# Kernel tuning notes

Hardware: AMD Instinct MI355X
Metric: run time of the kernel (lower is better)

Reference implementation:

```python
import jax, jax.numpy as jnp
import numpy as np

# Irrep dims for irreps 0e, 1o, 2e: 2l+1
IRREP_DIMS = (1, 3, 5)
B, N, C_IN, C_OUT = 8, 4096, 256, 256
FEAT = sum(IRREP_DIMS)  # 9


def setup_inputs() -> dict:
    key = jax.random.key(0)
    kx, k0, k1, k2 = jax.random.split(key, 4)
    std = C_IN ** -0.5  # VarianceScaling(fan_in) init
    return {
        "x": jax.random.normal(kx, (B, N, C_IN, FEAT), dtype=jnp.float32),
        "w0": jax.random.normal(k0, (C_IN, C_OUT), dtype=jnp.float32) * std,
        "w1": jax.random.normal(k1, (C_IN, C_OUT), dtype=jnp.float32) * std,
        "w2": jax.random.normal(k2, (C_IN, C_OUT), dtype=jnp.float32) * std,
    }


def reference(x, w0, w1, w2):
    # EquivariantLinear with mix_channels=True:
    #  - axis_to_mul merges the channel axis into irrep multiplicity, so each
    #    irrep block x[..., k, m] (k = channel/mul index, m = 2l+1 component)
    #    is contracted over k with a per-irrep weight w_l [mul_in, mul_out],
    #    scaled by path_weight = 1/sqrt(fan_in) (single path per output irrep).
    #  - mul_to_axis splits the multiplicity back into the channel axis.
    # Block-diagonal structure: one small matmul per matching irrep pair.
    mul_in = x.shape[-2]
    pw = jnp.asarray(mul_in, x.dtype) ** -0.5  # path_weight (1/sqrt fan_in)
    outs = []
    offset = 0
    for w, d in zip((w0, w1, w2), IRREP_DIMS):
        xl = jax.lax.slice_in_dim(x, offset, offset + d, axis=-1)  # [B,N,C,d]
        outs.append(pw * jnp.einsum('bnkm,kc->bncm', xl, w))
        offset += d
    return jnp.concatenate(outs, axis=-1)  # [B, N, C_out, 9]
```

## Files before the change

kernel.cpp:

```cpp
#include <hip/hip_runtime.h>


typedef float f32x4 __attribute__((ext_vector_type(4)));
typedef short s16x8 __attribute__((ext_vector_type(8)));

#define POSB 16
#define XS_KS 264
#define XS_MS (POSB * XS_KS)
#define SMEM_BYTES (9 * XS_MS * 2)
#define STG_ROW 148

__device__ __forceinline__ unsigned short f2bf(float f) {
  unsigned u = __float_as_uint(f);
  return (unsigned short)((u + 0x7FFFu + ((u >> 16) & 1u)) >> 16);
}

__global__ void prep_w(const float* __restrict__ w0, const float* __restrict__ w1,
                       const float* __restrict__ w2, unsigned short* __restrict__ wt) {
  const int b = blockIdx.x;
  const int irr = b / 16;
  const int tile = b % 16;
  const int k0 = (tile >> 2) << 6;
  const int c0 = (tile & 3) << 6;
  const float* w = (irr == 0) ? w0 : ((irr == 1) ? w1 : w2);
  __shared__ float lt[64 * 65];
  const int t = threadIdx.x;
#pragma unroll
  for (int i = 0; i < 16; ++i) {
    int e = t + (i << 8);
    int kk = e >> 6, cc = e & 63;
    lt[cc * 65 + kk] = w[(k0 + kk) * 256 + (c0 + cc)];
  }
  __syncthreads();
#pragma unroll
  for (int i = 0; i < 16; ++i) {
    int e = t + (i << 8);
    int cc = e >> 6, kk = e & 63;
    wt[irr * 65536 + (c0 + cc) * 256 + (k0 + kk)] = f2bf(lt[cc * 65 + kk] * 0.0625f);
  }
}

__global__ __launch_bounds__(512, 4) void eqlin_main(
    const float* __restrict__ x, const unsigned short* __restrict__ wt,
    float* __restrict__ out) {
  extern __shared__ char smem[];
  unsigned short* xs = reinterpret_cast<unsigned short*>(smem);

  const int t = threadIdx.x;
  const long long blk = blockIdx.x;
  const float* xb = x + blk * (POSB * 2304);

#pragma unroll
  for (int i = 0; i < 2; ++i) {
    const int p = t + (i << 9);
    const int pos = p >> 6;
    const int kq = (p & 63) << 2;
    const f32x4* src = reinterpret_cast<const f32x4*>(xb) + p * 9;
    float f[36];
#pragma unroll
    for (int j = 0; j < 9; ++j) {
      f32x4 v = src[j];
      f[j * 4 + 0] = v[0]; f[j * 4 + 1] = v[1];
      f[j * 4 + 2] = v[2]; f[j * 4 + 3] = v[3];
    }
#pragma unroll
    for (int m = 0; m < 9; ++m) {
      unsigned long long pk =
          (unsigned long long)f2bf(f[m]) |
          ((unsigned long long)f2bf(f[9 + m]) << 16) |
          ((unsigned long long)f2bf(f[18 + m]) << 32) |
          ((unsigned long long)f2bf(f[27 + m]) << 48);
      *reinterpret_cast<unsigned long long*>(xs + m * XS_MS + pos * XS_KS + kq) = pk;
    }
  }
  __syncthreads();

  const int w = t >> 6;
  const int l = t & 63;
  const int cr = l & 15;
  const int kg = (l >> 4) << 3;
  const int c0 = w << 5;

  const unsigned short* xsA = xs + cr * XS_KS + kg;
  const unsigned short* wtB = wt + (c0 + cr) * 256 + kg;

  f32x4 accA[4][2];
#pragma unroll
  for (int m = 0; m < 4; ++m)
#pragma unroll
    for (int ct = 0; ct < 2; ++ct) accA[m][ct] = (f32x4){0.f, 0.f, 0.f, 0.f};

#pragma unroll 2
  for (int ks = 0; ks < 8; ++ks) {
    const int kk = ks << 5;
    s16x8 b00 = *reinterpret_cast<const s16x8*>(wtB + kk);
    s16x8 b01 = *reinterpret_cast<const s16x8*>(wtB + 4096 + kk);
    s16x8 b10 = *reinterpret_cast<const s16x8*>(wtB + 65536 + kk);
    s16x8 b11 = *reinterpret_cast<const s16x8*>(wtB + 65536 + 4096 + kk);
    {
      s16x8 a = *reinterpret_cast<const s16x8*>(xsA + kk);
      accA[0][0] = __builtin_amdgcn_mfma_f32_16x16x32_bf16(a, b00, accA[0][0], 0, 0, 0);
      accA[0][1] = __builtin_amdgcn_mfma_f32_16x16x32_bf16(a, b01, accA[0][1], 0, 0, 0);
    }
#pragma unroll
    for (int m = 1; m < 4; ++m) {
      s16x8 a = *reinterpret_cast<const s16x8*>(xsA + m * XS_MS + kk);
      accA[m][0] = __builtin_amdgcn_mfma_f32_16x16x32_bf16(a, b10, accA[m][0], 0, 0, 0);
      accA[m][1] = __builtin_amdgcn_mfma_f32_16x16x32_bf16(a, b11, accA[m][1], 0, 0, 0);
    }
  }

  f32x4 accB[5][2];
#pragma unroll
  for (int m = 0; m < 5; ++m)
#pragma unroll
    for (int ct = 0; ct < 2; ++ct) accB[m][ct] = (f32x4){0.f, 0.f, 0.f, 0.f};

#pragma unroll 2
  for (int ks = 0; ks < 8; ++ks) {
    const int kk = ks << 5;
    s16x8 b20 = *reinterpret_cast<const s16x8*>(wtB + 2 * 65536 + kk);
    s16x8 b21 = *reinterpret_cast<const s16x8*>(wtB + 2 * 65536 + 4096 + kk);
#pragma unroll
    for (int m = 0; m < 5; ++m) {
      s16x8 a = *reinterpret_cast<const s16x8*>(xsA + (m + 4) * XS_MS + kk);
      accB[m][0] = __builtin_amdgcn_mfma_f32_16x16x32_bf16(a, b20, accB[m][0], 0, 0, 0);
      accB[m][1] = __builtin_amdgcn_mfma_f32_16x16x32_bf16(a, b21, accB[m][1], 0, 0, 0);
    }
  }
  __syncthreads();

  float* stgw = reinterpret_cast<float*>(smem) + w * (POSB * STG_ROW);
  const int posb = (l >> 4) << 2;
  f32x4* o4 = reinterpret_cast<f32x4*>(out) + blk * 9216 + w * 72;

#pragma unroll
  for (int ct = 0; ct < 2; ++ct) {
#pragma unroll
    for (int m = 0; m < 9; ++m) {
#pragma unroll
      for (int j = 0; j < 4; ++j) {
        float v = (m < 4) ? accA[m][ct][j] : accB[m - 4][ct][j];
        stgw[(posb + j) * STG_ROW + cr * 9 + m] = v;
      }
    }
    asm volatile("s_waitcnt lgkmcnt(0)" ::: "memory");
#pragma unroll
    for (int q = 0; q < 9; ++q) {
      const int e = l + (q << 6);
      const int pos = (int)((unsigned)e / 36u);
      const int rem = e - pos * 36;
      f32x4 v = *reinterpret_cast<const f32x4*>(stgw + pos * STG_ROW + (rem << 2));
      o4[pos * 576 + ct * 36 + rem] = v;
    }
    asm volatile("s_waitcnt lgkmcnt(0)" ::: "memory");
  }
}

extern "C" void kernel_launch(void* const* d_in, const int* in_sizes, int n_in,
                              void* d_out, int out_size, void* d_ws, size_t ws_size,
                              hipStream_t stream) {
  const float* x = (const float*)d_in[0];
  const float* w0 = (const float*)d_in[1];
  const float* w1 = (const float*)d_in[2];
  const float* w2 = (const float*)d_in[3];
  unsigned short* wt = (unsigned short*)d_ws;
  float* out = (float*)d_out;

  prep_w<<<48, 256, 0, stream>>>(w0, w1, w2, wt);

  (void)hipFuncSetAttribute(reinterpret_cast<const void*>(eqlin_main),
                            hipFuncAttributeMaxDynamicSharedMemorySize, SMEM_BYTES);
  eqlin_main<<<2048, 512, SMEM_BYTES, stream>>>(x, wt, out);
}
```

Before: 184.3 us.

## Make main kernel persistent with double-buffered LDS and register prefetch of next tile

Launches 256 blocks that each loop over 8 position tiles instead of 2048 one-shot blocks. The next tile's fp32 input is loaded into registers while the current tile is computed and stored, then converted to bf16 into an alternate LDS buffer. This aims to overlap global loads with MFMA work and output stores and to amortise per-block startup. It doubles LDS use per block and adds prefetch registers, lowering occupancy.

```diff
diff --git a/kernel.cpp b/kernel.cpp
--- a/kernel.cpp
+++ b/kernel.cpp
@@ -7,8 +7,10 @@
 #define POSB 16
 #define XS_KS 264
 #define XS_MS (POSB * XS_KS)
-#define SMEM_BYTES (9 * XS_MS * 2)
+#define BUF_BYTES (9 * XS_MS * 2)
+#define SMEM_BYTES (2 * BUF_BYTES)
 #define STG_ROW 148
+#define TILES_PER_BLK 8
 
 __device__ __forceinline__ unsigned short f2bf(float f) {
   unsigned u = __float_as_uint(f);
@@ -40,120 +42,150 @@
   }
 }
 
-__global__ __launch_bounds__(512, 4) void eqlin_main(
+__device__ __forceinline__ void stage_unit(unsigned short* xs, int pos, int kq,
+                                           const f32x4* pf) {
+#pragma unroll
+  for (int m = 0; m < 9; ++m) {
+    unsigned long long pk =
+        (unsigned long long)f2bf(pf[m >> 2][m & 3]) |
+        ((unsigned long long)f2bf(pf[(9 + m) >> 2][(9 + m) & 3]) << 16) |
+        ((unsigned long long)f2bf(pf[(18 + m) >> 2][(18 + m) & 3]) << 32) |
+        ((unsigned long long)f2bf(pf[(27 + m) >> 2][(27 + m) & 3]) << 48);
+    *reinterpret_cast<unsigned long long*>(xs + m * XS_MS + pos * XS_KS + kq) = pk;
+  }
+}
+
+__global__ __launch_bounds__(512, 2) void eqlin_main(
     const float* __restrict__ x, const unsigned short* __restrict__ wt,
     float* __restrict__ out) {
   extern __shared__ char smem[];
-  unsigned short* xs = reinterpret_cast<unsigned short*>(smem);
 
   const int t = threadIdx.x;
-  const long long blk = blockIdx.x;
-  const float* xb = x + blk * (POSB * 2304);
-
-#pragma unroll
-  for (int i = 0; i < 2; ++i) {
-    const int p = t + (i << 9);
-    const int pos = p >> 6;
-    const int kq = (p & 63) << 2;
-    const f32x4* src = reinterpret_cast<const f32x4*>(xb) + p * 9;
-    float f[36];
-#pragma unroll
-    for (int j = 0; j < 9; ++j) {
-      f32x4 v = src[j];
-      f[j * 4 + 0] = v[0]; f[j * 4 + 1] = v[1];
-      f[j * 4 + 2] = v[2]; f[j * 4 + 3] = v[3];
-    }
-#pragma unroll
-    for (int m = 0; m < 9; ++m) {
-      unsigned long long pk =
-          (unsigned long long)f2bf(f[m]) |
-          ((unsigned long long)f2bf(f[9 + m]) << 16) |
-          ((unsigned long long)f2bf(f[18 + m]) << 32) |
-          ((unsigned long long)f2bf(f[27 + m]) << 48);
-      *reinterpret_cast<unsigned long long*>(xs + m * XS_MS + pos * XS_KS + kq) = pk;
-    }
-  }
-  __syncthreads();
+
+  const int pos0 = t >> 6;
+  const int pos1 = pos0 + 8;
+  const int kq = (t & 63) << 2;
+  const int u0 = t * 9;
+  const int u1 = (t + 512) * 9;
+
+  const f32x4* xg = reinterpret_cast<const f32x4*>(x);
 
   const int w = t >> 6;
   const int l = t & 63;
   const int cr = l & 15;
   const int kg = (l >> 4) << 3;
   const int c0 = w << 5;
-
-  const unsigned short* xsA = xs + cr * XS_KS + kg;
   const unsigned short* wtB = wt + (c0 + cr) * 256 + kg;
 
-  f32x4 accA[4][2];
-#pragma unroll
-  for (int m = 0; m < 4; ++m)
-#pragma unroll
-    for (int ct = 0; ct < 2; ++ct) accA[m][ct] = (f32x4){0.f, 0.f, 0.f, 0.f};
+  const long long tile0 = (long long)blockIdx.x * TILES_PER_BLK;
+
+  f32x4 pfA[9], pfB[9];
+
+  {
+    const f32x4* s = xg + tile0 * 9216;
+#pragma unroll
+    for (int j = 0; j < 9; ++j) pfA[j] = s[u0 + j];
+#pragma unroll
+    for (int j = 0; j < 9; ++j) pfB[j] = s[u1 + j];
+    unsigned short* xs0 = reinterpret_cast<unsigned short*>(smem);
+    stage_unit(xs0, pos0, kq, pfA);
+    stage_unit(xs0, pos1, kq, pfB);
+  }
+  __syncthreads();
+
+  for (int it = 0; it < TILES_PER_BLK; ++it) {
+    const int p = it & 1;
+    const unsigned short* xsb =
+        reinterpret_cast<const unsigned short*>(smem + p * BUF_BYTES);
+
+    if (it + 1 < TILES_PER_BLK) {
+      const f32x4* s = xg + (tile0 + it + 1) * 9216;
+#pragma unroll
+      for (int j = 0; j < 9; ++j) pfA[j] = s[u0 + j];
+#pragma unroll
+      for (int j = 0; j < 9; ++j) pfB[j] = s[u1 + j];
+    }
+
+    const unsigned short* xsA = xsb + cr * XS_KS + kg;
+
+    f32x4 accA[4][2];
+#pragma unroll
+    for (int m = 0; m < 4; ++m)
+#pragma unroll
+      for (int ct = 0; ct < 2; ++ct) accA[m][ct] = (f32x4){0.f, 0.f, 0.f, 0.f};
 
 #pragma unroll 2
-  for (int ks = 0; ks < 8; ++ks) {
-    const int kk = ks << 5;
-    s16x8 b00 = *reinterpret_cast<const s16x8*>(wtB + kk);
-    s16x8 b01 = *reinterpret_cast<const s16x8*>(wtB + 4096 + kk);
-    s16x8 b10 = *reinterpret_cast<const s16x8*>(wtB + 65536 + kk);
-    s16x8 b11 = *reinterpret_cast<const s16x8*>(wtB + 65536 + 4096 + kk);
-    {
-      s16x8 a = *reinterpret_cast<const s16x8*>(xsA + kk);
-      accA[0][0] = __builtin_amdgcn_mfma_f32_16x16x32_bf16(a, b00, accA[0][0], 0, 0, 0);
-      accA[0][1] = __builtin_amdgcn_mfma_f32_16x16x32_bf16(a, b01, accA[0][1], 0, 0, 0);
-    }
-#pragma unroll
-    for (int m = 1; m < 4; ++m) {
-      s16x8 a = *reinterpret_cast<const s16x8*>(xsA + m * XS_MS + kk);
-      accA[m][0] = __builtin_amdgcn_mfma_f32_16x16x32_bf16(a, b10, accA[m][0], 0, 0, 0);
-      accA[m][1] = __builtin_amdgcn_mfma_f32_16x16x32_bf16(a, b11, accA[m][1], 0, 0, 0);
-    }
-  }
-
-  f32x4 accB[5][2];
-#pragma unroll
-  for (int m = 0; m < 5; ++m)
-#pragma unroll
-    for (int ct = 0; ct < 2; ++ct) accB[m][ct] = (f32x4){0.f, 0.f, 0.f, 0.f};
+    for (int ks = 0; ks < 8; ++ks) {
+      const int kk = ks << 5;
+      s16x8 b00 = *reinterpret_cast<const s16x8*>(wtB + kk);
+      s16x8 b01 = *reinterpret_cast<const s16x8*>(wtB + 4096 + kk);
+      s16x8 b10 = *reinterpret_cast<const s16x8*>(wtB + 65536 + kk);
+      s16x8 b11 = *reinterpret_cast<const s16x8*>(wtB + 65536 + 4096 + kk);
+      {
+        s16x8 a = *reinterpret_cast<const s16x8*>(xsA + kk);
+        accA[0][0] = __builtin_amdgcn_mfma_f32_16x16x32_bf16(a, b00, accA[0][0], 0, 0, 0);
+        accA[0][1] = __builtin_amdgcn_mfma_f32_16x16x32_bf16(a, b01, accA[0][1], 0, 0, 0);
+      }
+#pragma unroll
+      for (int m = 1; m < 4; ++m) {
+        s16x8 a = *reinterpret_cast<const s16x8*>(xsA + m * XS_MS + kk);
+        accA[m][0] = __builtin_amdgcn_mfma_f32_16x16x32_bf16(a, b10, accA[m][0], 0, 0, 0);
+        accA[m][1] = __builtin_amdgcn_mfma_f32_16x16x32_bf16(a, b11, accA[m][1], 0, 0, 0);
+      }
+    }
+
+    f32x4 accB[5][2];
+#pragma unroll
+    for (int m = 0; m < 5; ++m)
+#pragma unroll
+      for (int ct = 0; ct < 2; ++ct) accB[m][ct] = (f32x4){0.f, 0.f, 0.f, 0.f};
 
 #pragma unroll 2
-  for (int ks = 0; ks < 8; ++ks) {
-    const int kk = ks << 5;
-    s16x8 b20 = *reinterpret_cast<const s16x8*>(wtB + 2 * 65536 + kk);
-    s16x8 b21 = *reinterpret_cast<const s16x8*>(wtB + 2 * 65536 + 4096 + kk);
-#pragma unroll
-    for (int m = 0; m < 5; ++m) {
-      s16x8 a = *reinterpret_cast<const s16x8*>(xsA + (m + 4) * XS_MS + kk);
-      accB[m][0] = __builtin_amdgcn_mfma_f32_16x16x32_bf16(a, b20, accB[m][0], 0, 0, 0);
-      accB[m][1] = __builtin_amdgcn_mfma_f32_16x16x32_bf16(a, b21, accB[m][1], 0, 0, 0);
-    }
-  }
-  __syncthreads();
-
-  float* stgw = reinterpret_cast<float*>(smem) + w * (POSB * STG_ROW);
-  const int posb = (l >> 4) << 2;
-  f32x4* o4 = reinterpret_cast<f32x4*>(out) + blk * 9216 + w * 72;
-
-#pragma unroll
-  for (int ct = 0; ct < 2; ++ct) {
-#pragma unroll
-    for (int m = 0; m < 9; ++m) {
-#pragma unroll
-      for (int j = 0; j < 4; ++j) {
-        float v = (m < 4) ? accA[m][ct][j] : accB[m - 4][ct][j];
-        stgw[(posb + j) * STG_ROW + cr * 9 + m] = v;
-      }
-    }
-    asm volatile("s_waitcnt lgkmcnt(0)" ::: "memory");
-#pragma unroll
-    for (int q = 0; q < 9; ++q) {
-      const int e = l + (q << 6);
-      const int pos = (int)((unsigned)e / 36u);
-      const int rem = e - pos * 36;
-      f32x4 v = *reinterpret_cast<const f32x4*>(stgw + pos * STG_ROW + (rem << 2));
-      o4[pos * 576 + ct * 36 + rem] = v;
-    }
-    asm volatile("s_waitcnt lgkmcnt(0)" ::: "memory");
+    for (int ks = 0; ks < 8; ++ks) {
+      const int kk = ks << 5;
+      s16x8 b20 = *reinterpret_cast<const s16x8*>(wtB + 2 * 65536 + kk);
+      s16x8 b21 = *reinterpret_cast<const s16x8*>(wtB + 2 * 65536 + 4096 + kk);
+#pragma unroll
+      for (int m = 0; m < 5; ++m) {
+        s16x8 a = *reinterpret_cast<const s16x8*>(xsA + (m + 4) * XS_MS + kk);
+        accB[m][0] = __builtin_amdgcn_mfma_f32_16x16x32_bf16(a, b20, accB[m][0], 0, 0, 0);
+        accB[m][1] = __builtin_amdgcn_mfma_f32_16x16x32_bf16(a, b21, accB[m][1], 0, 0, 0);
+      }
+    }
+    __syncthreads();
+
+    float* stgw = reinterpret_cast<float*>(smem + p * BUF_BYTES) + w * (POSB * STG_ROW);
+    const int posb = (l >> 4) << 2;
+    f32x4* o4 = reinterpret_cast<f32x4*>(out) + (tile0 + it) * 9216 + w * 72;
+
+#pragma unroll
+    for (int ct = 0; ct < 2; ++ct) {
+#pragma unroll
+      for (int m = 0; m < 9; ++m) {
+#pragma unroll
+        for (int j = 0; j < 4; ++j) {
+          float v = (m < 4) ? accA[m][ct][j] : accB[m - 4][ct][j];
+          stgw[(posb + j) * STG_ROW + cr * 9 + m] = v;
+        }
+      }
+      asm volatile("s_waitcnt lgkmcnt(0)" ::: "memory");
+#pragma unroll
+      for (int q = 0; q < 9; ++q) {
+        const int e = l + (q << 6);
+        const int pos = (int)((unsigned)e / 36u);
+        const int rem = e - pos * 36;
+        f32x4 v = *reinterpret_cast<const f32x4*>(stgw + pos * STG_ROW + (rem << 2));
+        o4[pos * 576 + ct * 36 + rem] = v;
+      }
+      asm volatile("s_waitcnt lgkmcnt(0)" ::: "memory");
+    }
+
+    if (it + 1 < TILES_PER_BLK) {
+      unsigned short* xsn = reinterpret_cast<unsigned short*>(smem + (p ^ 1) * BUF_BYTES);
+      stage_unit(xsn, pos0, kq, pfA);
+      stage_unit(xsn, pos1, kq, pfB);
+    }
+    __syncthreads();
   }
 }
 
@@ -171,5 +203,5 @@
 
   (void)hipFuncSetAttribute(reinterpret_cast<const void*>(eqlin_main),
                             hipFuncAttributeMaxDynamicSharedMemorySize, SMEM_BYTES);
-  eqlin_main<<<2048, 512, SMEM_BYTES, stream>>>(x, wt, out);
-}
+  eqlin_main<<<256, 512, SMEM_BYTES, stream>>>(x, wt, out);
+}
```

New measurement: 211.2 us. +14.6%, slower.

## Pack 8-position M-tiles across irreps and split output channels over blocks

Applied to the files above, without the earlier changes.

Halves the positions per block to 8 and packs two irrep components into each 16-row MFMA tile, so 9 components need 6 MFMA tiles instead of 9 half-empty ones. Each block now handles half of the output channels, with the grid growing 4x and the launch-bound occupancy raised. Block indexing groups the two channel halves of a tile so they run close together and can share x in cache. The cost is that each x tile is loaded and converted twice, and the packing adds extra address logic.

```diff
diff --git a/kernel.cpp b/kernel.cpp
--- a/kernel.cpp
+++ b/kernel.cpp
@@ -4,7 +4,7 @@
 typedef float f32x4 __attribute__((ext_vector_type(4)));
 typedef short s16x8 __attribute__((ext_vector_type(8)));
 
-#define POSB 16
+#define POSB 8
 #define XS_KS 264
 #define XS_MS (POSB * XS_KS)
 #define SMEM_BYTES (9 * XS_MS * 2)
@@ -40,22 +40,25 @@
   }
 }
 
-__global__ __launch_bounds__(512, 4) void eqlin_main(
+__global__ __launch_bounds__(512, 6) void eqlin_main(
     const float* __restrict__ x, const unsigned short* __restrict__ wt,
     float* __restrict__ out) {
   extern __shared__ char smem[];
   unsigned short* xs = reinterpret_cast<unsigned short*>(smem);
 
   const int t = threadIdx.x;
-  const long long blk = blockIdx.x;
-  const float* xb = x + blk * (POSB * 2304);
+  const int b = blockIdx.x;
+  const int grp = b >> 4;
+  const int sub = b & 15;
+  const int tile = (grp << 3) | (sub & 7);
+  const int chalf = sub >> 3;
 
-#pragma unroll
-  for (int i = 0; i < 2; ++i) {
-    const int p = t + (i << 9);
-    const int pos = p >> 6;
-    const int kq = (p & 63) << 2;
-    const f32x4* src = reinterpret_cast<const f32x4*>(xb) + p * 9;
+  const float* xb = x + (long long)tile * (POSB * 2304);
+
+  {
+    const int pos = t >> 6;
+    const int kq = (t & 63) << 2;
+    const f32x4* src = reinterpret_cast<const f32x4*>(xb) + t * 9;
     float f[36];
 #pragma unroll
     for (int j = 0; j < 9; ++j) {
@@ -79,81 +82,74 @@
   const int l = t & 63;
   const int cr = l & 15;
   const int kg = (l >> 4) << 3;
-  const int c0 = w << 5;
+  const int cb = chalf * 128 + (w << 4);
 
-  const unsigned short* xsA = xs + cr * XS_KS + kg;
-  const unsigned short* wtB = wt + (c0 + cr) * 256 + kg;
+  const unsigned short* wtB = wt + (cb + cr) * 256 + kg;
 
-  f32x4 accA[4][2];
+  const bool hi = (cr >= 8);
+  const unsigned short* xrow = xs + (cr & 7) * XS_KS + kg;
+  const unsigned short* xa[6] = {
+      xrow + 0 * XS_MS,
+      xrow + (hi ? 2 : 1) * XS_MS,
+      xrow + 3 * XS_MS,
+      xrow + (hi ? 5 : 4) * XS_MS,
+      xrow + (hi ? 7 : 6) * XS_MS,
+      xrow + 8 * XS_MS,
+  };
+
+  f32x4 acc[6];
 #pragma unroll
-  for (int m = 0; m < 4; ++m)
+  for (int T = 0; T < 6; ++T) acc[T] = (f32x4){0.f, 0.f, 0.f, 0.f};
+
 #pragma unroll
-    for (int ct = 0; ct < 2; ++ct) accA[m][ct] = (f32x4){0.f, 0.f, 0.f, 0.f};
-
-#pragma unroll 2
   for (int ks = 0; ks < 8; ++ks) {
     const int kk = ks << 5;
-    s16x8 b00 = *reinterpret_cast<const s16x8*>(wtB + kk);
-    s16x8 b01 = *reinterpret_cast<const s16x8*>(wtB + 4096 + kk);
-    s16x8 b10 = *reinterpret_cast<const s16x8*>(wtB + 65536 + kk);
-    s16x8 b11 = *reinterpret_cast<const s16x8*>(wtB + 65536 + 4096 + kk);
-    {
-      s16x8 a = *reinterpret_cast<const s16x8*>(xsA + kk);
-      accA[0][0] = __builtin_amdgcn_mfma_f32_16x16x32_bf16(a, b00, accA[0][0], 0, 0, 0);
-      accA[0][1] = __builtin_amdgcn_mfma_f32_16x16x32_bf16(a, b01, accA[0][1], 0, 0, 0);
-    }
-#pragma unroll
-    for (int m = 1; m < 4; ++m) {
-      s16x8 a = *reinterpret_cast<const s16x8*>(xsA + m * XS_MS + kk);
-      accA[m][0] = __builtin_amdgcn_mfma_f32_16x16x32_bf16(a, b10, accA[m][0], 0, 0, 0);
-      accA[m][1] = __builtin_amdgcn_mfma_f32_16x16x32_bf16(a, b11, accA[m][1], 0, 0, 0);
-    }
-  }
-
-  f32x4 accB[5][2];
-#pragma unroll
-  for (int m = 0; m < 5; ++m)
-#pragma unroll
-    for (int ct = 0; ct < 2; ++ct) accB[m][ct] = (f32x4){0.f, 0.f, 0.f, 0.f};
-
-#pragma unroll 2
-  for (int ks = 0; ks < 8; ++ks) {
-    const int kk = ks << 5;
-    s16x8 b20 = *reinterpret_cast<const s16x8*>(wtB + 2 * 65536 + kk);
-    s16x8 b21 = *reinterpret_cast<const s16x8*>(wtB + 2 * 65536 + 4096 + kk);
-#pragma unroll
-    for (int m = 0; m < 5; ++m) {
-      s16x8 a = *reinterpret_cast<const s16x8*>(xsA + (m + 4) * XS_MS + kk);
-      accB[m][0] = __builtin_amdgcn_mfma_f32_16x16x32_bf16(a, b20, accB[m][0], 0, 0, 0);
-      accB[m][1] = __builtin_amdgcn_mfma_f32_16x16x32_bf16(a, b21, accB[m][1], 0, 0, 0);
-    }
+    s16x8 b0 = *reinterpret_cast<const s16x8*>(wtB + kk);
+    s16x8 b1 = *reinterpret_cast<const s16x8*>(wtB + 65536 + kk);
+    s16x8 b2 = *reinterpret_cast<const s16x8*>(wtB + 131072 + kk);
+    s16x8 a0 = *reinterpret_cast<const s16x8*>(xa[0] + kk);
+    acc[0] = __builtin_amdgcn_mfma_f32_16x16x32_bf16(a0, b0, acc[0], 0, 0, 0);
+    s16x8 a1 = *reinterpret_cast<const s16x8*>(xa[1] + kk);
+    acc[1] = __builtin_amdgcn_mfma_f32_16x16x32_bf16(a1, b1, acc[1], 0, 0, 0);
+    s16x8 a2 = *reinterpret_cast<const s16x8*>(xa[2] + kk);
+    acc[2] = __builtin_amdgcn_mfma_f32_16x16x32_bf16(a2, b1, acc[2], 0, 0, 0);
+    s16x8 a3 = *reinterpret_cast<const s16x8*>(xa[3] + kk);
+    acc[3] = __builtin_amdgcn_mfma_f32_16x16x32_bf16(a3, b2, acc[3], 0, 0, 0);
+    s16x8 a4 = *reinterpret_cast<const s16x8*>(xa[4] + kk);
+    acc[4] = __builtin_amdgcn_mfma_f32_16x16x32_bf16(a4, b2, acc[4], 0, 0, 0);
+    s16x8 a5 = *reinterpret_cast<const s16x8*>(xa[5] + kk);
+    acc[5] = __builtin_amdgcn_mfma_f32_16x16x32_bf16(a5, b2, acc[5], 0, 0, 0);
   }
   __syncthreads();
 
   float* stgw = reinterpret_cast<float*>(smem) + w * (POSB * STG_ROW);
-  const int posb = (l >> 4) << 2;
-  f32x4* o4 = reinterpret_cast<f32x4*>(out) + blk * 9216 + w * 72;
+  const int gq = l >> 4;
+  const int jb = (gq & 1) << 2;
 
+  const int pAt[6] = {0, 1, 3, 4, 6, 8};
+  const int pBt[6] = {0, 2, 3, 5, 7, 8};
 #pragma unroll
-  for (int ct = 0; ct < 2; ++ct) {
+  for (int T = 0; T < 6; ++T) {
+    const int m = (gq < 2) ? pAt[T] : pBt[T];
+    if (gq < 2 || pAt[T] != pBt[T]) {
 #pragma unroll
-    for (int m = 0; m < 9; ++m) {
+      for (int j = 0; j < 4; ++j)
+        stgw[(jb + j) * STG_ROW + cr * 9 + m] = acc[T][j];
+    }
+  }
+  asm volatile("s_waitcnt lgkmcnt(0)" ::: "memory");
+
+  const long long obase = (long long)tile * (POSB * 576) + chalf * 288 + w * 36;
+  f32x4* o4 = reinterpret_cast<f32x4*>(out);
 #pragma unroll
-      for (int j = 0; j < 4; ++j) {
-        float v = (m < 4) ? accA[m][ct][j] : accB[m - 4][ct][j];
-        stgw[(posb + j) * STG_ROW + cr * 9 + m] = v;
-      }
-    }
-    asm volatile("s_waitcnt lgkmcnt(0)" ::: "memory");
-#pragma unroll
-    for (int q = 0; q < 9; ++q) {
-      const int e = l + (q << 6);
+  for (int q = 0; q < 5; ++q) {
+    const int e = l + (q << 6);
+    if (e < 288) {
       const int pos = (int)((unsigned)e / 36u);
       const int rem = e - pos * 36;
       f32x4 v = *reinterpret_cast<const f32x4*>(stgw + pos * STG_ROW + (rem << 2));
-      o4[pos * 576 + ct * 36 + rem] = v;
+      o4[obase + (long long)pos * 576 + rem] = v;
     }
-    asm volatile("s_waitcnt lgkmcnt(0)" ::: "memory");
   }
 }
 
@@ -171,5 +167,5 @@
 
   (void)hipFuncSetAttribute(reinterpret_cast<const void*>(eqlin_main),
                             hipFuncAttributeMaxDynamicSharedMemorySize, SMEM_BYTES);
-  eqlin_main<<<2048, 512, SMEM_BYTES, stream>>>(x, wt, out);
+  eqlin_main<<<8192, 512, SMEM_BYTES, stream>>>(x, wt, out);
 }
```

New measurement: 265.5 us. 44.0% more time.
